# Kernel tuning notes

Hardware: AMD Instinct MI355X
Metric: run time of the kernel (lower is better)

## Reference

```python
import jax, jax.numpy as jnp
import numpy as np

B, V, N, H, S = 16, 3, 512, 512, 5  # batch, vec (PDE system size), grid points, MLP hidden, stencil
DT_DX = 0.1
OFFSETS = (-2, -1, 0, 1, 2)


def setup_inputs() -> dict:
    key = jax.random.key(0)
    ks = jax.random.split(key, 4)
    scale1 = 1.0 / np.sqrt(V * S)
    scale2 = 1.0 / np.sqrt(H)
    return {
        "initial_state": jax.random.normal(ks[0], (B, V, N), dtype=jnp.float32),
        "W1": jax.random.normal(ks[1], (V * S, H), dtype=jnp.float32) * scale1,
        "b1": jnp.zeros((H,), dtype=jnp.float32),
        "W2": jax.random.normal(ks[2], (H, H), dtype=jnp.float32) * scale2,
        "b2": jnp.zeros((H,), dtype=jnp.float32),
        "W3": jax.random.normal(ks[3], (H, S), dtype=jnp.float32) * scale2,
        "b3": jnp.zeros((S,), dtype=jnp.float32),
        "num_steps": 32,
    }


def _cell(u, W1, b1, W2, b2, W3, b3):
    """IntegrateCell: stencil -> policy MLP -> flux weights -> conservative update.
    u: [B, V, N]. Returns (action [B,N,S], reward [B,N], next_state [B,V,N])."""
    # periodic 5-point stencil: stencil[..., k] = u[i + OFFSETS[k]]
    stencil = jnp.stack([jnp.roll(u, -o, axis=-1) for o in OFFSETS], axis=-1)  # [B,V,N,S]
    feats = stencil.transpose(0, 2, 1, 3).reshape(B, N, V * S)  # [B,N,V*S]
    h = jnp.tanh(feats @ W1 + b1)
    h = jnp.tanh(h @ W2 + b2)
    logits = h @ W3 + b3  # [B,N,S]
    w = jax.nn.softmax(logits, axis=-1)  # convex stencil weights (the action)
    flux = jnp.einsum("bvns,bns->bvn", stencil, w)  # numerical flux at interfaces
    next_u = u - DT_DX * (flux - jnp.roll(flux, 1, axis=-1))  # conservative update
    reward = -jnp.sum(jnp.square(w), axis=-1)  # [B,N] per-location reward
    return w, reward, next_u


def reference(initial_state, W1, b1, W2, b2, W3, b3, num_steps):
    def step(u, _):
        action, reward, next_u = _cell(u, W1, b1, W2, b2, W3, b3)
        return next_u, (next_u, action, reward)

    _final, (states, actions, rewards) = jax.lax.scan(
        step, initial_state, None, length=num_steps)
    # states: [T,B,V,N]; actions: [T,B,N,S]; rewards: [T,B,N]
    # (spatial_dims=1, so actions/rewards tuples in the TF code have one element each)
    return states, actions, rewards
```

## Files before the change

### kernel.cpp

```cpp
#include <hip/hip_runtime.h>
#include <hip/hip_bf16.h>

typedef __attribute__((ext_vector_type(8))) short short8;
typedef __attribute__((ext_vector_type(4))) float f32x4;

#define BB 16
#define VV 3
#define NN 512
#define SS 5
#define TT 32
#define DTDX 0.1f

#define GLOAD_LDS16(g, l)                                          \
  __builtin_amdgcn_global_load_lds(                                \
      (const __attribute__((address_space(1))) void*)(g),          \
      (__attribute__((address_space(3))) void*)(l), 16, 0, 0)

__device__ __forceinline__ float fast_tanh(float x) {
  float xc = fminf(fmaxf(x, -9.f), 9.f);
  float e = __expf(2.f * xc);
  return (e - 1.f) * __builtin_amdgcn_rcpf(e + 1.f);
}

__device__ __forceinline__ short f2bf(float x) {
  __hip_bfloat16 h = __float2bfloat16(x);
  return __builtin_bit_cast(short, h);
}

__global__ void init_repack(const float* __restrict__ W1,
                            const float* __restrict__ b1,
                            const float* __restrict__ W2,
                            const float* __restrict__ W3,
                            short* __restrict__ W1F,
                            short* __restrict__ W2F,
                            short* __restrict__ W3F) {
  const int blk = blockIdx.x;
  const int tid = threadIdx.x;
  if (blk < 128) {
    const int fid = blk * 256 + tid;
    const int lane = fid & 63;
    const int rest = fid >> 6;
    const int ks = rest & 15;
    const int ct = rest >> 4;
    const int col = ct * 16 + (lane & 15);
    const int k0 = ks * 32 + (lane >> 4) * 8;
    short8 v;
#pragma unroll
    for (int q = 0; q < 8; ++q) v[q] = f2bf(W2[(size_t)(k0 + q) * 512 + col]);
    *(short8*)(W2F + (size_t)fid * 8) = v;
  } else if (blk < 132) {
    const int fid = (blk - 128) * 256 + tid;
    const int lane = fid & 63;
    const int ks = fid >> 6;
    const int ml = lane & 15;
    const int k0 = ks * 32 + (lane >> 4) * 8;
    short8 v;
#pragma unroll
    for (int q = 0; q < 8; ++q)
      v[q] = f2bf((ml < 5) ? W3[(size_t)(k0 + q) * 5 + ml] : 0.f);
    *(short8*)(W3F + (size_t)fid * 8) = v;
  } else {
    for (int fid = tid; fid < 2048; fid += 256) {
      const int lane = fid & 63;
      const int nt = fid >> 6;
      const int col = nt * 16 + (lane & 15);
      const int k0 = (lane >> 4) * 8;
      short8 v;
#pragma unroll
      for (int q = 0; q < 8; ++q) {
        const int k = k0 + q;
        float x = 0.f;
        if (k < 15) x = W1[(size_t)k * 512 + col];
        else if (k == 15) x = b1[col];
        v[q] = f2bf(x);
      }
      *(short8*)(W1F + (size_t)fid * 8) = v;
    }
  }
}

template <bool FIRST>
__global__ __launch_bounds__(1024, 4) void step_kernel(
    const float* __restrict__ u_prev, const float* __restrict__ flux_prev,
    const short* __restrict__ W1F, const short* __restrict__ W2F,
    const float* __restrict__ b2, const short* __restrict__ W3F,
    const float* __restrict__ b3, float* __restrict__ u_out,
    float* __restrict__ states_out, float* __restrict__ flux_out,
    float* __restrict__ actions_out, float* __restrict__ rewards_out) {
  __shared__ float u_lds[VV][40];
  __shared__ __align__(16) short h_lds[32 * 512];
  __shared__ __align__(16) short ring[16 * 3 * 1024];
  __shared__ float logits_lds[32][16];

  const int tid = threadIdx.x;
  const int blk = blockIdx.x;
  const int b = blk >> 4;
  const int n0 = (blk & 15) << 5;

  const int lane = tid & 63;
  const int wv = tid >> 6;
  const int ml = lane & 15;
  const int gg = lane >> 4;
  const int aswz = ml << 3;
  const int ct0 = wv * 2;
  short* const rb = ring + wv * 3072;

#define ISSUE_SLOT(ks2)                                                       \
  do {                                                                        \
    const int _s = (ks2) % 3;                                                 \
    GLOAD_LDS16(W2F + ((size_t)(ct0 * 16 + (ks2)) * 64 + lane) * 8,           \
                rb + _s * 1024);                                              \
    GLOAD_LDS16(W2F + ((size_t)((ct0 + 1) * 16 + (ks2)) * 64 + lane) * 8,     \
                rb + _s * 1024 + 512);                                        \
  } while (0)

  ISSUE_SLOT(0);
  ISSUE_SLOT(1);

  if (tid < 108) {
    const int v = tid / 36;
    const int i = tid - v * 36;
    const int n = (n0 - 2 + i) & (NN - 1);
    const int base = (b * VV + v) * NN;
    const int gi = base + n;
    float uv;
    if (FIRST) {
      uv = u_prev[gi];
    } else {
      const int nm = (n - 1) & (NN - 1);
      uv = u_prev[gi] - DTDX * (flux_prev[base + n] - flux_prev[base + nm]);
      if (i >= 2 && i < 34) {
        u_out[gi] = uv;
        states_out[gi] = uv;
      }
    }
    u_lds[v][i] = uv;
  }
  __syncthreads();

  {
    const short8 wb0 = *(const short8*)(W1F + ((size_t)ct0 * 64 + lane) * 8);
    const short8 wb1 =
        *(const short8*)(W1F + ((size_t)(ct0 + 1) * 64 + lane) * 8);
    short8 afr[2];
#pragma unroll
    for (int mt = 0; mt < 2; ++mt) {
      const int r = mt * 16 + ml;
      short8 a;
#pragma unroll
      for (int q = 0; q < 8; ++q) a[q] = 0;
      if (gg == 0) {
#pragma unroll
        for (int q = 0; q < 8; ++q) {
          const int v = q / 5, s = q % 5;
          a[q] = f2bf(u_lds[v][r + s]);
        }
      } else if (gg == 1) {
#pragma unroll
        for (int q = 0; q < 7; ++q) {
          const int k = 8 + q;
          const int v = k / 5, s = k % 5;
          a[q] = f2bf(u_lds[v][r + s]);
        }
        a[7] = f2bf(1.0f);
      }
      afr[mt] = a;
    }
    f32x4 c[2][2];
#pragma unroll
    for (int mt = 0; mt < 2; ++mt)
#pragma unroll
      for (int nt = 0; nt < 2; ++nt) c[mt][nt] = (f32x4){0.f, 0.f, 0.f, 0.f};
    c[0][0] = __builtin_amdgcn_mfma_f32_16x16x32_bf16(afr[0], wb0, c[0][0], 0, 0, 0);
    c[1][0] = __builtin_amdgcn_mfma_f32_16x16x32_bf16(afr[1], wb0, c[1][0], 0, 0, 0);
    c[0][1] = __builtin_amdgcn_mfma_f32_16x16x32_bf16(afr[0], wb1, c[0][1], 0, 0, 0);
    c[1][1] = __builtin_amdgcn_mfma_f32_16x16x32_bf16(afr[1], wb1, c[1][1], 0, 0, 0);
#pragma unroll
    for (int nt = 0; nt < 2; ++nt) {
      const int col = (ct0 + nt) * 16 + ml;
#pragma unroll
      for (int mt = 0; mt < 2; ++mt) {
#pragma unroll
        for (int r = 0; r < 4; ++r) {
          const int row = mt * 16 + gg * 4 + r;
          h_lds[row * 512 + (col ^ ((row & 15) << 3))] =
              f2bf(fast_tanh(c[mt][nt][r]));
        }
      }
    }
  }
  __syncthreads();

  f32x4 acc[2][2];
#pragma unroll
  for (int mt = 0; mt < 2; ++mt)
#pragma unroll
    for (int nt = 0; nt < 2; ++nt) acc[mt][nt] = (f32x4){0.f, 0.f, 0.f, 0.f};

#pragma unroll
  for (int ks = 0; ks < 16; ++ks) {
    if (ks < 14) {
      ISSUE_SLOT(ks + 2);
      asm volatile("s_waitcnt vmcnt(4)" ::: "memory");
    } else if (ks == 14) {
      asm volatile("s_waitcnt vmcnt(2)" ::: "memory");
    } else {
      asm volatile("s_waitcnt vmcnt(0)" ::: "memory");
    }
    const int slot = ks % 3;
    const int k = ks * 32 + gg * 8;
    const short8 a0 = *(const short8*)(&h_lds[ml * 512 + (k ^ aswz)]);
    const short8 a1 = *(const short8*)(&h_lds[(16 + ml) * 512 + (k ^ aswz)]);
    const short8 b0 = *(const short8*)(rb + slot * 1024 + lane * 8);
    const short8 b1v = *(const short8*)(rb + slot * 1024 + 512 + lane * 8);
    __builtin_amdgcn_s_setprio(1);
    acc[0][0] = __builtin_amdgcn_mfma_f32_16x16x32_bf16(a0, b0, acc[0][0], 0, 0, 0);
    acc[1][0] = __builtin_amdgcn_mfma_f32_16x16x32_bf16(a1, b0, acc[1][0], 0, 0, 0);
    acc[0][1] = __builtin_amdgcn_mfma_f32_16x16x32_bf16(a0, b1v, acc[0][1], 0, 0, 0);
    acc[1][1] = __builtin_amdgcn_mfma_f32_16x16x32_bf16(a1, b1v, acc[1][1], 0, 0, 0);
    __builtin_amdgcn_s_setprio(0);
  }
#undef ISSUE_SLOT
  __syncthreads();

#pragma unroll
  for (int nt = 0; nt < 2; ++nt) {
    const int col = (ct0 + nt) * 16 + ml;
    const float bias = b2[col];
#pragma unroll
    for (int mt = 0; mt < 2; ++mt) {
#pragma unroll
      for (int r = 0; r < 4; ++r) {
        const int row = mt * 16 + gg * 4 + r;
        h_lds[row * 512 + (col ^ ((row & 15) << 3))] =
            f2bf(fast_tanh(acc[mt][nt][r] + bias));
      }
    }
  }
  __syncthreads();

  if (wv < 2) {
    f32x4 a3 = (f32x4){0.f, 0.f, 0.f, 0.f};
    const short8* B3p = (const short8*)W3F;
#pragma unroll 4
    for (int ks = 0; ks < 16; ++ks) {
      const int k = ks * 32 + gg * 8;
      const short8 a =
          *(const short8*)(&h_lds[(wv * 16 + ml) * 512 + (k ^ aswz)]);
      const short8 bb = B3p[ks * 64 + lane];
      a3 = __builtin_amdgcn_mfma_f32_16x16x32_bf16(a, bb, a3, 0, 0, 0);
    }
#pragma unroll
    for (int r = 0; r < 4; ++r) logits_lds[wv * 16 + gg * 4 + r][ml] = a3[r];
  }
  __syncthreads();

  if (tid < 32) {
    const int r = tid;
    const int n = n0 + r;
    float lg[5];
#pragma unroll
    for (int s = 0; s < 5; ++s) lg[s] = logits_lds[r][s] + b3[s];
    const float m =
        fmaxf(fmaxf(fmaxf(lg[0], lg[1]), fmaxf(lg[2], lg[3])), lg[4]);
    float e[5], sum = 0.f;
#pragma unroll
    for (int s = 0; s < 5; ++s) {
      e[s] = __expf(lg[s] - m);
      sum += e[s];
    }
    const float inv = 1.f / sum;
    float w[5], rw = 0.f;
#pragma unroll
    for (int s = 0; s < 5; ++s) {
      w[s] = e[s] * inv;
      rw += w[s] * w[s];
    }
    float* ap = actions_out + ((size_t)b * NN + n) * SS;
#pragma unroll
    for (int s = 0; s < 5; ++s) ap[s] = w[s];
    rewards_out[b * NN + n] = -rw;
#pragma unroll
    for (int v = 0; v < VV; ++v) {
      float fx = 0.f;
#pragma unroll
      for (int s = 0; s < 5; ++s) fx += u_lds[v][r + s] * w[s];
      flux_out[(b * VV + v) * NN + n] = fx;
    }
  }
}

__global__ void final_update(const float* __restrict__ u_prev,
                             const float* __restrict__ flux_prev,
                             float* __restrict__ states_out) {
  const int idx = blockIdx.x * 256 + threadIdx.x;
  if (idx < BB * VV * NN) {
    const int n = idx & (NN - 1);
    const int base = idx - n;
    const int nm = (n - 1) & (NN - 1);
    states_out[idx] =
        u_prev[idx] - DTDX * (flux_prev[idx] - flux_prev[base + nm]);
  }
}

extern "C" void kernel_launch(void* const* d_in, const int* in_sizes, int n_in,
                              void* d_out, int out_size, void* d_ws,
                              size_t ws_size, hipStream_t stream) {
  const float* u0 = (const float*)d_in[0];
  const float* W1 = (const float*)d_in[1];
  const float* b1 = (const float*)d_in[2];
  const float* W2 = (const float*)d_in[3];
  const float* b2 = (const float*)d_in[4];
  const float* W3 = (const float*)d_in[5];
  const float* b3 = (const float*)d_in[6];

  float* states = (float*)d_out;
  float* actions = states + (size_t)TT * BB * VV * NN;
  float* rewards = actions + (size_t)TT * BB * NN * SS;

  char* ws = (char*)d_ws;
  float* ubuf[2] = {(float*)ws, (float*)(ws + 98304)};
  float* fbuf[2] = {(float*)(ws + 2 * 98304), (float*)(ws + 3 * 98304)};
  short* W1F = (short*)(ws + 4 * 98304);
  short* W2F = (short*)(ws + 4 * 98304 + 32768);
  short* W3F = (short*)(ws + 4 * 98304 + 32768 + 524288);

  init_repack<<<dim3(133), dim3(256), 0, stream>>>(W1, b1, W2, W3, W1F, W2F,
                                                   W3F);

  for (int t = 0; t < TT; ++t) {
    if (t == 0) {
      step_kernel<true><<<dim3(256), dim3(1024), 0, stream>>>(
          u0, (const float*)nullptr, W1F, W2F, b2, W3F, b3, (float*)nullptr,
          (float*)nullptr, fbuf[0], actions, rewards);
    } else {
      const float* up = (t == 1) ? u0 : ubuf[(t - 1) & 1];
      step_kernel<false><<<dim3(256), dim3(1024), 0, stream>>>(
          up, fbuf[(t - 1) & 1], W1F, W2F, b2, W3F, b3, ubuf[t & 1],
          states + (size_t)(t - 1) * BB * VV * NN, fbuf[t & 1],
          actions + (size_t)t * BB * NN * SS, rewards + (size_t)t * BB * NN);
    }
  }
  final_update<<<dim3((BB * VV * NN + 255) / 256), dim3(256), 0, stream>>>(
      ubuf[1], fbuf[1], states + (size_t)(TT - 1) * BB * VV * NN);
}
```

Baseline: 376.9 us.

## Split W3 GEMM across all waves with K-partial reduction; hoist W1 loads

The third-layer GEMM (hidden to 5 logits) previously ran on only 2 waves doing 16 MFMA steps each. It is now split across all 16 waves: each wave handles one row half and a 2-step K chunk. The partial sums go to a small shared buffer and are reduced by the softmax threads. W1 fragment loads are also hoisted above the first barrier so they overlap the stencil setup, and output stores for states, actions and rewards use nontemporal hints. The extra reduction pass over shared memory adds a little work to the serial tail.

```diff
diff --git a/kernel.cpp b/kernel.cpp
--- a/kernel.cpp
+++ b/kernel.cpp
@@ -90,7 +90,7 @@
   __shared__ float u_lds[VV][40];
   __shared__ __align__(16) short h_lds[32 * 512];
   __shared__ __align__(16) short ring[16 * 3 * 1024];
-  __shared__ float logits_lds[32][16];
+  __shared__ float part_lds[8][32][6];
 
   const int tid = threadIdx.x;
   const int blk = blockIdx.x;
@@ -116,6 +116,10 @@
 
   ISSUE_SLOT(0);
   ISSUE_SLOT(1);
+
+  const short8 wb0 = *(const short8*)(W1F + ((size_t)ct0 * 64 + lane) * 8);
+  const short8 wb1 =
+      *(const short8*)(W1F + ((size_t)(ct0 + 1) * 64 + lane) * 8);
 
   if (tid < 108) {
     const int v = tid / 36;
@@ -131,7 +135,7 @@
       uv = u_prev[gi] - DTDX * (flux_prev[base + n] - flux_prev[base + nm]);
       if (i >= 2 && i < 34) {
         u_out[gi] = uv;
-        states_out[gi] = uv;
+        __builtin_nontemporal_store(uv, states_out + gi);
       }
     }
     u_lds[v][i] = uv;
@@ -139,9 +143,6 @@
   __syncthreads();
 
   {
-    const short8 wb0 = *(const short8*)(W1F + ((size_t)ct0 * 64 + lane) * 8);
-    const short8 wb1 =
-        *(const short8*)(W1F + ((size_t)(ct0 + 1) * 64 + lane) * 8);
     short8 afr[2];
 #pragma unroll
     for (int mt = 0; mt < 2; ++mt) {
@@ -239,19 +240,25 @@
   }
   __syncthreads();
 
-  if (wv < 2) {
+  {
+    const int kc = wv >> 1;
+    const int rh = wv & 1;
     f32x4 a3 = (f32x4){0.f, 0.f, 0.f, 0.f};
     const short8* B3p = (const short8*)W3F;
-#pragma unroll 4
-    for (int ks = 0; ks < 16; ++ks) {
+#pragma unroll
+    for (int j = 0; j < 2; ++j) {
+      const int ks = kc * 2 + j;
       const int k = ks * 32 + gg * 8;
       const short8 a =
-          *(const short8*)(&h_lds[(wv * 16 + ml) * 512 + (k ^ aswz)]);
+          *(const short8*)(&h_lds[(rh * 16 + ml) * 512 + (k ^ aswz)]);
       const short8 bb = B3p[ks * 64 + lane];
       a3 = __builtin_amdgcn_mfma_f32_16x16x32_bf16(a, bb, a3, 0, 0, 0);
     }
-#pragma unroll
-    for (int r = 0; r < 4; ++r) logits_lds[wv * 16 + gg * 4 + r][ml] = a3[r];
+    if (ml < 5) {
+#pragma unroll
+      for (int r = 0; r < 4; ++r)
+        part_lds[kc][rh * 16 + gg * 4 + r][ml] = a3[r];
+    }
   }
   __syncthreads();
 
@@ -260,7 +267,12 @@
     const int n = n0 + r;
     float lg[5];
 #pragma unroll
-    for (int s = 0; s < 5; ++s) lg[s] = logits_lds[r][s] + b3[s];
+    for (int s = 0; s < 5; ++s) {
+      float a = b3[s];
+#pragma unroll
+      for (int kc = 0; kc < 8; ++kc) a += part_lds[kc][r][s];
+      lg[s] = a;
+    }
     const float m =
         fmaxf(fmaxf(fmaxf(lg[0], lg[1]), fmaxf(lg[2], lg[3])), lg[4]);
     float e[5], sum = 0.f;
@@ -278,8 +290,8 @@
     }
     float* ap = actions_out + ((size_t)b * NN + n) * SS;
 #pragma unroll
-    for (int s = 0; s < 5; ++s) ap[s] = w[s];
-    rewards_out[b * NN + n] = -rw;
+    for (int s = 0; s < 5; ++s) __builtin_nontemporal_store(w[s], ap + s);
+    __builtin_nontemporal_store(-rw, rewards_out + b * NN + n);
 #pragma unroll
     for (int v = 0; v < VV; ++v) {
       float fx = 0.f;
```

Result: no change. 379.2 us (+0.6%).
